# Kernel tuning notes

Hardware: AMD Instinct MI355X
Metric: run time of the kernel (lower is better)

## Reference

```python
import jax, jax.numpy as jnp
import numpy as np

EMBED_DIM = 1024
NUM_HEADS = 16
HEAD_DIM = EMBED_DIM // NUM_HEADS
B, S = 2, 2048
BIG = 1e9  # clamp / nan_to_num saturation value from the torch module


def setup_inputs() -> dict:
    key = jax.random.key(0)
    k1, k2, k3, k4, k5 = jax.random.split(key, 5)
    sc = 1.0 / np.sqrt(EMBED_DIM)
    x = jax.random.normal(k1, (B, S, EMBED_DIM), dtype=jnp.float32)
    qkv_w = jax.random.normal(k2, (3 * EMBED_DIM, EMBED_DIM), dtype=jnp.float32) * sc
    qkv_b = jax.random.normal(k3, (3 * EMBED_DIM,), dtype=jnp.float32) * 0.01
    out_w = jax.random.normal(k4, (EMBED_DIM, EMBED_DIM), dtype=jnp.float32) * sc
    out_b = jax.random.normal(k5, (EMBED_DIM,), dtype=jnp.float32) * 0.01
    # causal mask, broadcastable to [B, H, S, S]; 0 => masked
    mask = jnp.tril(jnp.ones((S, S), dtype=jnp.int32))[None, None, :, :]
    return {"x": x, "mask": mask, "qkv_w": qkv_w, "qkv_b": qkv_b,
            "out_w": out_w, "out_b": out_b}


def reference(x, mask, qkv_w, qkv_b, out_w, out_b):
    b, s, e = x.shape
    # fused QKV projection (torch Linear: x @ W.T + b)
    qkv = x @ qkv_w.T + qkv_b                      # [B, S, 3E]
    q, k, v = jnp.split(qkv, 3, axis=-1)
    def heads(t):
        return t.reshape(b, s, NUM_HEADS, HEAD_DIM).transpose(0, 2, 1, 3)  # [B,H,S,D]
    q, k, v = heads(q), heads(k), heads(v)
    scores = jnp.einsum('bhqd,bhkd->bhqk', q, k) / np.sqrt(HEAD_DIM)
    scores = jnp.clip(scores, -BIG, BIG)
    # masked_fill(mask==0, -inf) then nan_to_num(neginf=-1e9) => masked -> -1e9
    scores = jnp.where(mask == 0, -jnp.inf, scores)
    scores = jnp.nan_to_num(scores, nan=0.0, posinf=BIG, neginf=-BIG)
    scores = scores - jnp.max(scores, axis=-1, keepdims=True)
    attn = jax.nn.softmax(scores, axis=-1) + 1e-9
    out = jnp.einsum('bhqk,bhkd->bhqd', attn, v)   # [B,H,S,D]
    out = out.transpose(0, 2, 1, 3).reshape(b, s, e)
    return out @ out_w.T + out_b
```

## Files before the change

kernel.cpp:

```cpp
#include <hip/hip_runtime.h>
#include <stdint.h>

#define B_ 2
#define H_ 16
#define S_ 2048
#define D_ 64
#define E_ 1024
#define M_ 4096
#define N3_ 3072

typedef __attribute__((ext_vector_type(8))) short bf16x8;
typedef __attribute__((ext_vector_type(4))) float f32x4;
typedef __attribute__((ext_vector_type(16))) float f32x16;
typedef __attribute__((ext_vector_type(4))) unsigned short us4;
typedef __attribute__((ext_vector_type(4))) int i32x4;

__device__ __forceinline__ unsigned short f2b(float f) {
  union { float f; unsigned int u; } v; v.f = f;
  unsigned int r = v.u + 0x7FFFu + ((v.u >> 16) & 1u);
  return (unsigned short)(r >> 16);
}

__device__ __forceinline__ void gll16(const void* g, void* l) {
  __builtin_amdgcn_global_load_lds((const __attribute__((address_space(1))) uint32_t*)g,
                                   (__attribute__((address_space(3))) uint32_t*)l, 16, 0, 0);
}

__global__ __launch_bounds__(256)
void f32_to_bf16_3(const float* __restrict__ a, const float* __restrict__ b,
                   const float* __restrict__ c,
                   unsigned short* __restrict__ oa, unsigned short* __restrict__ ob,
                   unsigned short* __restrict__ oc) {
  int i = (blockIdx.x * blockDim.x + threadIdx.x) * 4;
  const float* src; unsigned short* dst; int j;
  if (i < 4194304)      { src = a; dst = oa; j = i; }
  else if (i < 7340032) { src = b; dst = ob; j = i - 4194304; }
  else                  { src = c; dst = oc; j = i - 7340032; }
  float4 v = *(const float4*)(src + j);
  us4 o; o.x = f2b(v.x); o.y = f2b(v.y); o.z = f2b(v.z); o.w = f2b(v.w);
  *(us4*)(dst + j) = o;
}

template<int MODE>
__global__ __launch_bounds__(512)
void gemm_bt_k(const unsigned short* __restrict__ A,
               const unsigned short* __restrict__ Bw,
               const float* __restrict__ bias,
               float* __restrict__ outf,
               unsigned short* __restrict__ qo,
               unsigned short* __restrict__ ko,
               unsigned short* __restrict__ vto,
               const int K) {
  __shared__ unsigned short As[2][128 * 32];
  __shared__ unsigned short Bs[2][128 * 32];
  const int tid = threadIdx.x;
  const int wid = tid >> 6, lane = tid & 63;
  const int l4 = lane & 15, lh = lane >> 4;
  const int gx = gridDim.x;
  int id = blockIdx.y * gx + blockIdx.x;
  const int cpx = (gx * gridDim.y) >> 3;
  id = (id & 7) * cpx + (id >> 3);
  const int bm = (id / gx) << 7, bn = (id % gx) << 7;
  const int mq = wid >> 2, nq = wid & 3;
  const int wm = mq << 6, wn = nq << 5;
  f32x4 acc[4][2] = {};
  const int srow = lane >> 2;
  const int scolb = ((lane & 3) ^ (((lane >> 3) & 1) << 1)) << 4;
  auto STAGE = [&](int bb, int kt) {
    const int r = (wid << 4) + srow;
    gll16((const char*)A + ((size_t)(bm + r) * K + kt) * 2 + scolb, &As[bb][wid << 9]);
    gll16((const char*)Bw + ((size_t)(bn + r) * K + kt) * 2 + scolb, &Bs[bb][wid << 9]);
  };
  const int NT = K >> 5;
  STAGE(0, 0);
  STAGE(1, 32);
  asm volatile("s_waitcnt vmcnt(2)" ::: "memory");
  __builtin_amdgcn_s_barrier();
  asm volatile("" ::: "memory");
  const int ro = (l4 << 5) + ((lh ^ (((l4 >> 1) & 1) << 1)) << 3);
  for (int t = 0; t < NT; ++t) {
    const int bb = t & 1;
    bf16x8 af[4], bfr[2];
#pragma unroll
    for (int g = 0; g < 4; ++g)
      af[g] = *(const bf16x8*)&As[bb][(((mq << 2) + g) << 9) + ro];
#pragma unroll
    for (int h = 0; h < 2; ++h)
      bfr[h] = *(const bf16x8*)&Bs[bb][(((nq << 1) + h) << 9) + ro];
#pragma unroll
    for (int mg = 0; mg < 4; ++mg)
#pragma unroll
      for (int ng = 0; ng < 2; ++ng)
        acc[mg][ng] = __builtin_amdgcn_mfma_f32_16x16x32_bf16(af[mg], bfr[ng], acc[mg][ng], 0, 0, 0);
    asm volatile("s_waitcnt lgkmcnt(0)" ::: "memory");
    __builtin_amdgcn_s_barrier();
    if (t < NT - 2) {
      STAGE(bb, (t + 2) << 5);
      asm volatile("s_waitcnt vmcnt(2)" ::: "memory");
    } else {
      asm volatile("s_waitcnt vmcnt(0)" ::: "memory");
    }
    __builtin_amdgcn_s_barrier();
    asm volatile("" ::: "memory");
  }
#pragma unroll
  for (int mg = 0; mg < 4; ++mg) {
#pragma unroll
    for (int ng = 0; ng < 2; ++ng) {
      const int n = bn + wn + (ng << 4) + l4;
      const float bv = bias[n];
      const int m0 = bm + wm + (mg << 4) + (lh << 2);
      if (MODE == 1) {
#pragma unroll
        for (int i = 0; i < 4; ++i)
          outf[(size_t)(m0 + i) * E_ + n] = acc[mg][ng][i] + bv;
      } else {
        const int region = n >> 10;
        const int nn = n & 1023;
        const int h = nn >> 6, d = nn & 63;
        const int b = m0 >> 11, s0 = m0 & 2047;
        const int bh = (b << 4) + h;
        if (region == 2) {
          us4 pk;
#pragma unroll
          for (int i = 0; i < 4; ++i) pk[i] = f2b(acc[mg][ng][i] + bv);
          *(us4*)&vto[((size_t)bh * D_ + d) * S_ + s0] = pk;
        } else {
          unsigned short* dst = (region == 0) ? qo : ko;
          const float sc = (region == 0) ? 0.125f : 1.0f;
#pragma unroll
          for (int i = 0; i < 4; ++i)
            dst[((size_t)bh * S_ + s0 + i) * D_ + d] = f2b((acc[mg][ng][i] + bv) * sc);
        }
      }
    }
  }
}

__global__ __launch_bounds__(512)
void attn_k(const unsigned short* __restrict__ Q,
            const unsigned short* __restrict__ Kt,
            const unsigned short* __restrict__ Vt,
            unsigned short* __restrict__ O) {
  __shared__ __align__(16) char smem[65536];
  const int tid = threadIdx.x;
  const int wid = tid >> 6, lane = tid & 63;
  const int l31 = lane & 31, hi = lane >> 5, hi4 = hi << 2;
  const int bid = blockIdx.x;
  const int xcd = bid & 7, jj = bid >> 3;
  const int bh = (xcd << 2) + (jj & 3);
  const int pairq = jj >> 2;
  const int qbB = 15 - pairq;
  const int myqb = (wid < 4) ? pairq : qbB;
  const int q0w = (myqb << 7) + ((wid & 3) << 5);
  const int npair = qbB + 1;
  const int ntaw = ((q0w + 31) >> 6) + 1;

  const char* Qb = (const char*)Q + (size_t)bh * (S_ * D_ * 2);
  const char* Kb = (const char*)Kt + (size_t)bh * (S_ * D_ * 2);
  const char* Vb = (const char*)Vt + (size_t)bh * (D_ * S_ * 2);

  bf16x8 qf[4];
#pragma unroll
  for (int st = 0; st < 4; ++st)
    qf[st] = *(const bf16x8*)(Qb + (size_t)(q0w + l31) * 128 + (st << 5) + (hi << 4));

  const int sw = wid & 3;
  const int r1 = (sw << 4) + (lane >> 3), r2 = r1 + 8;
  const int cc = lane & 7;
  const int ko1 = (r1 << 7) + ((cc ^ (r1 & 7)) << 4);
  const int ko2 = (r2 << 7) + ((cc ^ (r2 & 7)) << 4);
  const int vo1 = (r1 << 12) + ((cc ^ (r1 & 7)) << 4);
  const int vo2 = (r2 << 12) + ((cc ^ (r2 & 7)) << 4);

  f32x16 oacc[2] = {};
  float m_i = -3.0e38f, l_i = 0.0f;
  const int qg = q0w + l31;
  const int swl = l31 & 7;

  auto STAGEP = [&](int b, int tk) {
    const int sub = tk & 1;
    char* kd = smem + (b << 14) + (sub << 13) + (sw << 11);
    char* vd = smem + 32768 + (b << 14) + (sub << 13) + (sw << 11);
    if (wid < 4) {
      gll16(Kb + (size_t)tk * 8192 + ko1, kd);
      gll16(Kb + (size_t)tk * 8192 + ko2, kd + 1024);
    } else {
      gll16(Vb + (size_t)tk * 128 + vo1, vd);
      gll16(Vb + (size_t)tk * 128 + vo2, vd + 1024);
    }
  };

  STAGEP(0, 0); STAGEP(0, 1);
  __syncthreads();

  for (int tp = 0; tp < npair; ++tp) {
    const int cur = tp & 1;
    if (tp + 1 < npair) {
      STAGEP(cur ^ 1, (tp << 1) + 2);
      STAGEP(cur ^ 1, (tp << 1) + 3);
    }
#pragma unroll
    for (int sub = 0; sub < 2; ++sub) {
      const int tk = (tp << 1) + sub;
      if (tk >= ntaw) break;
      const char* Kc = smem + (cur << 14) + (sub << 13);
      const char* Vc = smem + 32768 + (cur << 14) + (sub << 13);
      f32x16 sacc[2] = {};
#pragma unroll
      for (int tt = 0; tt < 2; ++tt)
#pragma unroll
        for (int st = 0; st < 4; ++st) {
          bf16x8 kf = *(const bf16x8*)(Kc + (tt << 12) + (l31 << 7) + ((((st << 1) + hi) ^ swl) << 4));
          sacc[tt] = __builtin_amdgcn_mfma_f32_32x32x16_bf16(kf, qf[st], sacc[tt], 0, 0, 0);
        }
      if (tk == ntaw - 1) {
        const int kv0 = tk << 6;
#pragma unroll
        for (int tt = 0; tt < 2; ++tt)
#pragma unroll
          for (int r = 0; r < 16; ++r) {
            const int kg = kv0 + (tt << 5) + (r & 3) + ((r >> 2) << 3) + hi4;
            if (kg > qg) sacc[tt][r] = -3.0e38f;
          }
      }
      float pmax = -3.0e38f;
#pragma unroll
      for (int tt = 0; tt < 2; ++tt)
#pragma unroll
        for (int r = 0; r < 16; ++r) pmax = fmaxf(pmax, sacc[tt][r]);
      pmax = fmaxf(pmax, __shfl_xor(pmax, 32));
      if (__any(pmax > m_i + 8.0f)) {
        const float mn = fmaxf(m_i, pmax);
        const float scl = __expf(m_i - mn);
        l_i *= scl;
        m_i = mn;
#pragma unroll
        for (int r = 0; r < 16; ++r) {
          const float sr = __shfl(scl, (r & 3) + ((r >> 2) << 3) + hi4);
          oacc[0][r] *= sr;
          oacc[1][r] *= sr;
        }
      }
#pragma unroll
      for (int tt = 0; tt < 2; ++tt)
#pragma unroll
        for (int r = 0; r < 16; ++r) {
          const float p = __expf(sacc[tt][r] - m_i);
          l_i += p;
          sacc[tt][r] = p;
        }
#pragma unroll
      for (int ks = 0; ks < 4; ++ks) {
        const int tt = ks >> 1, r0 = (ks & 1) << 3;
        int w0, w1, w2, w3;
        asm("v_cvt_pk_bf16_f32 %0, %1, %2" : "=v"(w0) : "v"(sacc[tt][r0 + 0]), "v"(sacc[tt][r0 + 1]));
        asm("v_cvt_pk_bf16_f32 %0, %1, %2" : "=v"(w1) : "v"(sacc[tt][r0 + 2]), "v"(sacc[tt][r0 + 3]));
        asm("v_cvt_pk_bf16_f32 %0, %1, %2" : "=v"(w2) : "v"(sacc[tt][r0 + 4]), "v"(sacc[tt][r0 + 5]));
        asm("v_cvt_pk_bf16_f32 %0, %1, %2" : "=v"(w3) : "v"(sacc[tt][r0 + 6]), "v"(sacc[tt][r0 + 7]));
        asm("v_permlane32_swap_b32 %0, %1" : "+v"(w0), "+v"(w2));
        asm("v_permlane32_swap_b32 %0, %1" : "+v"(w1), "+v"(w3));
        union { i32x4 i; bf16x8 h; } u;
        u.i.x = w0; u.i.y = w1; u.i.z = w2; u.i.w = w3;
        const bf16x8 pa = u.h;
#pragma unroll
        for (int dt = 0; dt < 2; ++dt) {
          bf16x8 vf = *(const bf16x8*)(Vc + (dt << 12) + (l31 << 7) + ((((ks << 1) + hi) ^ swl) << 4));
          oacc[dt] = __builtin_amdgcn_mfma_f32_32x32x16_bf16(pa, vf, oacc[dt], 0, 0, 0);
        }
      }
    }
    __syncthreads();
  }

  const float ltot = l_i + __shfl_xor(l_i, 32);
  const float inv = 1.0f / ltot;
  const int b = bh >> 4, h = bh & 15;
#pragma unroll
  for (int r = 0; r < 16; ++r) {
    const int qr = (r & 3) + ((r >> 2) << 3) + hi4;
    const float ivr = __shfl(inv, qr);
    const size_t off = ((size_t)((b << 11) + q0w + qr) << 10) + (h << 6) + l31;
    O[off]      = f2b(oacc[0][r] * ivr);
    O[off + 32] = f2b(oacc[1][r] * ivr);
  }
}

extern "C" void kernel_launch(void* const* d_in, const int* in_sizes, int n_in,
                              void* d_out, int out_size, void* d_ws, size_t ws_size,
                              hipStream_t stream) {
  const float* x     = (const float*)d_in[0];
  const float* qkv_w = (const float*)d_in[2];
  const float* qkv_b = (const float*)d_in[3];
  const float* out_w = (const float*)d_in[4];
  const float* out_b = (const float*)d_in[5];

  unsigned short* ws   = (unsigned short*)d_ws;
  unsigned short* xb   = ws;
  unsigned short* wqkv = xb + (size_t)M_ * E_;
  unsigned short* wout = wqkv + (size_t)N3_ * E_;
  unsigned short* qB   = wout + (size_t)E_ * E_;
  unsigned short* kB   = qB + (size_t)32 * S_ * D_;
  unsigned short* vtB  = kB + (size_t)32 * S_ * D_;
  unsigned short* oB   = ws;

  f32_to_bf16_3<<<8192, 256, 0, stream>>>(x, qkv_w, out_w, xb, wqkv, wout);

  gemm_bt_k<0><<<dim3(N3_ / 128, M_ / 128), 512, 0, stream>>>(
      xb, wqkv, qkv_b, nullptr, qB, kB, vtB, E_);

  attn_k<<<256, 512, 0, stream>>>(qB, kB, vtB, oB);

  gemm_bt_k<1><<<dim3(E_ / 128, M_ / 128), 512, 0, stream>>>(
      oB, wout, out_b, (float*)d_out, nullptr, nullptr, nullptr, E_);
}
```

Before: 106.1 us.

## Store Q/K/V in MFMA-fragment order and load attention operands directly from global

The QKV GEMM epilogue now writes Q, K and V^T in a pre-swizzled fragment layout, so each lane's bf16x8 MFMA operand is a contiguous 16-byte chunk. The attention kernel drops its LDS double-buffering and barriers and reads K/V fragments straight from global/L2 into registers. Blocks shrink to 4 waves with a new per-wave query-tile schedule (heaviest first). This removes LDS traffic and sync costs, but loses cross-wave K/V sharing in LDS and raises register pressure, with K/V loads no longer overlapped with compute by explicit prefetch.

```diff
diff --git a/kernel.cpp b/kernel.cpp
--- a/kernel.cpp
+++ b/kernel.cpp
@@ -124,153 +124,130 @@
           us4 pk;
 #pragma unroll
           for (int i = 0; i < 4; ++i) pk[i] = f2b(acc[mg][ng][i] + bv);
-          *(us4*)&vto[((size_t)bh * D_ + d) * S_ + s0] = pk;
+          const size_t ev = ((size_t)bh << 17) + ((size_t)(s0 >> 6) << 12) + ((d >> 5) << 11)
+                          + (((s0 >> 4) & 3) << 9) + (((s0 >> 3) & 1) << 8)
+                          + ((d & 31) << 3) + (s0 & 7);
+          *(us4*)&vto[ev] = pk;
         } else {
           unsigned short* dst = (region == 0) ? qo : ko;
           const float sc = (region == 0) ? 0.125f : 1.0f;
 #pragma unroll
-          for (int i = 0; i < 4; ++i)
-            dst[((size_t)bh * S_ + s0 + i) * D_ + d] = f2b((acc[mg][ng][i] + bv) * sc);
+          for (int i = 0; i < 4; ++i) {
+            const int s = s0 + i;
+            const size_t e = ((size_t)bh << 17) + ((size_t)(s >> 6) << 12) + (((s >> 5) & 1) << 11)
+                           + ((d >> 4) << 9) + (((d >> 3) & 1) << 8)
+                           + ((s & 31) << 3) + (d & 7);
+            dst[e] = f2b((acc[mg][ng][i] + bv) * sc);
+          }
         }
       }
     }
   }
 }
 
-__global__ __launch_bounds__(512)
-void attn_k(const unsigned short* __restrict__ Q,
-            const unsigned short* __restrict__ Kt,
-            const unsigned short* __restrict__ Vt,
+__global__ __launch_bounds__(256)
+void attn_k(const unsigned short* __restrict__ QF,
+            const unsigned short* __restrict__ KF,
+            const unsigned short* __restrict__ VF,
             unsigned short* __restrict__ O) {
-  __shared__ __align__(16) char smem[65536];
   const int tid = threadIdx.x;
   const int wid = tid >> 6, lane = tid & 63;
   const int l31 = lane & 31, hi = lane >> 5, hi4 = hi << 2;
   const int bid = blockIdx.x;
-  const int xcd = bid & 7, jj = bid >> 3;
-  const int bh = (xcd << 2) + (jj & 3);
-  const int pairq = jj >> 2;
-  const int qbB = 15 - pairq;
-  const int myqb = (wid < 4) ? pairq : qbB;
-  const int q0w = (myqb << 7) + ((wid & 3) << 5);
-  const int npair = qbB + 1;
-  const int ntaw = ((q0w + 31) >> 6) + 1;
-
-  const char* Qb = (const char*)Q + (size_t)bh * (S_ * D_ * 2);
-  const char* Kb = (const char*)Kt + (size_t)bh * (S_ * D_ * 2);
-  const char* Vb = (const char*)Vt + (size_t)bh * (D_ * S_ * 2);
+  const int bh = ((bid & 7) << 2) + ((bid >> 3) & 3);
+  const int qi = 63 - (((bid >> 5) << 2) + wid);
+  const int q0 = qi << 5;
+  const int ntaw = (qi >> 1) + 1;
+
+  const char* Qb = (const char*)QF + ((size_t)bh << 18);
+  const char* Kb = (const char*)KF + ((size_t)bh << 18);
+  const char* Vb = (const char*)VF + ((size_t)bh << 18);
 
   bf16x8 qf[4];
-#pragma unroll
-  for (int st = 0; st < 4; ++st)
-    qf[st] = *(const bf16x8*)(Qb + (size_t)(q0w + l31) * 128 + (st << 5) + (hi << 4));
-
-  const int sw = wid & 3;
-  const int r1 = (sw << 4) + (lane >> 3), r2 = r1 + 8;
-  const int cc = lane & 7;
-  const int ko1 = (r1 << 7) + ((cc ^ (r1 & 7)) << 4);
-  const int ko2 = (r2 << 7) + ((cc ^ (r2 & 7)) << 4);
-  const int vo1 = (r1 << 12) + ((cc ^ (r1 & 7)) << 4);
-  const int vo2 = (r2 << 12) + ((cc ^ (r2 & 7)) << 4);
+  {
+    const char* qc = Qb + ((size_t)(qi >> 1) << 13) + ((qi & 1) << 12) + lane * 16;
+#pragma unroll
+    for (int st = 0; st < 4; ++st)
+      qf[st] = *(const bf16x8*)(qc + (st << 10));
+  }
 
   f32x16 oacc[2] = {};
   float m_i = -3.0e38f, l_i = 0.0f;
-  const int qg = q0w + l31;
-  const int swl = l31 & 7;
-
-  auto STAGEP = [&](int b, int tk) {
-    const int sub = tk & 1;
-    char* kd = smem + (b << 14) + (sub << 13) + (sw << 11);
-    char* vd = smem + 32768 + (b << 14) + (sub << 13) + (sw << 11);
-    if (wid < 4) {
-      gll16(Kb + (size_t)tk * 8192 + ko1, kd);
-      gll16(Kb + (size_t)tk * 8192 + ko2, kd + 1024);
-    } else {
-      gll16(Vb + (size_t)tk * 128 + vo1, vd);
-      gll16(Vb + (size_t)tk * 128 + vo2, vd + 1024);
-    }
-  };
-
-  STAGEP(0, 0); STAGEP(0, 1);
-  __syncthreads();
-
-  for (int tp = 0; tp < npair; ++tp) {
-    const int cur = tp & 1;
-    if (tp + 1 < npair) {
-      STAGEP(cur ^ 1, (tp << 1) + 2);
-      STAGEP(cur ^ 1, (tp << 1) + 3);
-    }
-#pragma unroll
-    for (int sub = 0; sub < 2; ++sub) {
-      const int tk = (tp << 1) + sub;
-      if (tk >= ntaw) break;
-      const char* Kc = smem + (cur << 14) + (sub << 13);
-      const char* Vc = smem + 32768 + (cur << 14) + (sub << 13);
-      f32x16 sacc[2] = {};
+  const int qg = q0 + l31;
+
+  for (int t = 0; t < ntaw; ++t) {
+    const char* Kc = Kb + ((size_t)t << 13) + lane * 16;
+    const char* Vc = Vb + ((size_t)t << 13) + lane * 16;
+    bf16x8 kf[2][4], vf[2][4];
+#pragma unroll
+    for (int tt = 0; tt < 2; ++tt)
+#pragma unroll
+      for (int st = 0; st < 4; ++st)
+        kf[tt][st] = *(const bf16x8*)(Kc + (tt << 12) + (st << 10));
+#pragma unroll
+    for (int dt = 0; dt < 2; ++dt)
+#pragma unroll
+      for (int ks = 0; ks < 4; ++ks)
+        vf[dt][ks] = *(const bf16x8*)(Vc + (dt << 12) + (ks << 10));
+    f32x16 sacc[2] = {};
+#pragma unroll
+    for (int tt = 0; tt < 2; ++tt)
+#pragma unroll
+      for (int st = 0; st < 4; ++st)
+        sacc[tt] = __builtin_amdgcn_mfma_f32_32x32x16_bf16(kf[tt][st], qf[st], sacc[tt], 0, 0, 0);
+    if (t == ntaw - 1) {
+      const int kv0 = t << 6;
 #pragma unroll
       for (int tt = 0; tt < 2; ++tt)
 #pragma unroll
-        for (int st = 0; st < 4; ++st) {
-          bf16x8 kf = *(const bf16x8*)(Kc + (tt << 12) + (l31 << 7) + ((((st << 1) + hi) ^ swl) << 4));
-          sacc[tt] = __builtin_amdgcn_mfma_f32_32x32x16_bf16(kf, qf[st], sacc[tt], 0, 0, 0);
+        for (int r = 0; r < 16; ++r) {
+          const int kg = kv0 + (tt << 5) + (r & 3) + ((r >> 2) << 3) + hi4;
+          if (kg > qg) sacc[tt][r] = -3.0e38f;
         }
-      if (tk == ntaw - 1) {
-        const int kv0 = tk << 6;
-#pragma unroll
-        for (int tt = 0; tt < 2; ++tt)
-#pragma unroll
-          for (int r = 0; r < 16; ++r) {
-            const int kg = kv0 + (tt << 5) + (r & 3) + ((r >> 2) << 3) + hi4;
-            if (kg > qg) sacc[tt][r] = -3.0e38f;
-          }
+    }
+    float pmax = -3.0e38f;
+#pragma unroll
+    for (int tt = 0; tt < 2; ++tt)
+#pragma unroll
+      for (int r = 0; r < 16; ++r) pmax = fmaxf(pmax, sacc[tt][r]);
+    pmax = fmaxf(pmax, __shfl_xor(pmax, 32));
+    if (__any(pmax > m_i + 8.0f)) {
+      const float mn = fmaxf(m_i, pmax);
+      const float scl = __expf(m_i - mn);
+      l_i *= scl;
+      m_i = mn;
+#pragma unroll
+      for (int r = 0; r < 16; ++r) {
+        const float sr = __shfl(scl, (r & 3) + ((r >> 2) << 3) + hi4);
+        oacc[0][r] *= sr;
+        oacc[1][r] *= sr;
       }
-      float pmax = -3.0e38f;
-#pragma unroll
-      for (int tt = 0; tt < 2; ++tt)
-#pragma unroll
-        for (int r = 0; r < 16; ++r) pmax = fmaxf(pmax, sacc[tt][r]);
-      pmax = fmaxf(pmax, __shfl_xor(pmax, 32));
-      if (__any(pmax > m_i + 8.0f)) {
-        const float mn = fmaxf(m_i, pmax);
-        const float scl = __expf(m_i - mn);
-        l_i *= scl;
-        m_i = mn;
-#pragma unroll
-        for (int r = 0; r < 16; ++r) {
-          const float sr = __shfl(scl, (r & 3) + ((r >> 2) << 3) + hi4);
-          oacc[0][r] *= sr;
-          oacc[1][r] *= sr;
-        }
+    }
+#pragma unroll
+    for (int tt = 0; tt < 2; ++tt)
+#pragma unroll
+      for (int r = 0; r < 16; ++r) {
+        const float p = __expf(sacc[tt][r] - m_i);
+        l_i += p;
+        sacc[tt][r] = p;
       }
 #pragma unroll
-      for (int tt = 0; tt < 2; ++tt)
-#pragma unroll
-        for (int r = 0; r < 16; ++r) {
-          const float p = __expf(sacc[tt][r] - m_i);
-          l_i += p;
-          sacc[tt][r] = p;
-        }
-#pragma unroll
-      for (int ks = 0; ks < 4; ++ks) {
-        const int tt = ks >> 1, r0 = (ks & 1) << 3;
-        int w0, w1, w2, w3;
-        asm("v_cvt_pk_bf16_f32 %0, %1, %2" : "=v"(w0) : "v"(sacc[tt][r0 + 0]), "v"(sacc[tt][r0 + 1]));
-        asm("v_cvt_pk_bf16_f32 %0, %1, %2" : "=v"(w1) : "v"(sacc[tt][r0 + 2]), "v"(sacc[tt][r0 + 3]));
-        asm("v_cvt_pk_bf16_f32 %0, %1, %2" : "=v"(w2) : "v"(sacc[tt][r0 + 4]), "v"(sacc[tt][r0 + 5]));
-        asm("v_cvt_pk_bf16_f32 %0, %1, %2" : "=v"(w3) : "v"(sacc[tt][r0 + 6]), "v"(sacc[tt][r0 + 7]));
-        asm("v_permlane32_swap_b32 %0, %1" : "+v"(w0), "+v"(w2));
-        asm("v_permlane32_swap_b32 %0, %1" : "+v"(w1), "+v"(w3));
-        union { i32x4 i; bf16x8 h; } u;
-        u.i.x = w0; u.i.y = w1; u.i.z = w2; u.i.w = w3;
-        const bf16x8 pa = u.h;
-#pragma unroll
-        for (int dt = 0; dt < 2; ++dt) {
-          bf16x8 vf = *(const bf16x8*)(Vc + (dt << 12) + (l31 << 7) + ((((ks << 1) + hi) ^ swl) << 4));
-          oacc[dt] = __builtin_amdgcn_mfma_f32_32x32x16_bf16(pa, vf, oacc[dt], 0, 0, 0);
-        }
-      }
-    }
-    __syncthreads();
+    for (int ks = 0; ks < 4; ++ks) {
+      const int tt = ks >> 1, r0 = (ks & 1) << 3;
+      int w0, w1, w2, w3;
+      asm("v_cvt_pk_bf16_f32 %0, %1, %2" : "=v"(w0) : "v"(sacc[tt][r0 + 0]), "v"(sacc[tt][r0 + 1]));
+      asm("v_cvt_pk_bf16_f32 %0, %1, %2" : "=v"(w1) : "v"(sacc[tt][r0 + 2]), "v"(sacc[tt][r0 + 3]));
+      asm("v_cvt_pk_bf16_f32 %0, %1, %2" : "=v"(w2) : "v"(sacc[tt][r0 + 4]), "v"(sacc[tt][r0 + 5]));
+      asm("v_cvt_pk_bf16_f32 %0, %1, %2" : "=v"(w3) : "v"(sacc[tt][r0 + 6]), "v"(sacc[tt][r0 + 7]));
+      asm("v_permlane32_swap_b32 %0, %1" : "+v"(w0), "+v"(w2));
+      asm("v_permlane32_swap_b32 %0, %1" : "+v"(w1), "+v"(w3));
+      union { i32x4 i; bf16x8 h; } u;
+      u.i.x = w0; u.i.y = w1; u.i.z = w2; u.i.w = w3;
+      const bf16x8 pa = u.h;
+#pragma unroll
+      for (int dt = 0; dt < 2; ++dt)
+        oacc[dt] = __builtin_amdgcn_mfma_f32_32x32x16_bf16(pa, vf[dt][ks], oacc[dt], 0, 0, 0);
+    }
   }
 
   const float ltot = l_i + __shfl_xor(l_i, 32);
@@ -280,7 +257,7 @@
   for (int r = 0; r < 16; ++r) {
     const int qr = (r & 3) + ((r >> 2) << 3) + hi4;
     const float ivr = __shfl(inv, qr);
-    const size_t off = ((size_t)((b << 11) + q0w + qr) << 10) + (h << 6) + l31;
+    const size_t off = ((size_t)((b << 11) + q0 + qr) << 10) + (h << 6) + l31;
     O[off]      = f2b(oacc[0][r] * ivr);
     O[off + 32] = f2b(oacc[1][r] * ivr);
   }
@@ -309,7 +286,7 @@
   gemm_bt_k<0><<<dim3(N3_ / 128, M_ / 128), 512, 0, stream>>>(
       xb, wqkv, qkv_b, nullptr, qB, kB, vtB, E_);
 
-  attn_k<<<256, 512, 0, stream>>>(qB, kB, vtB, oB);
+  attn_k<<<512, 256, 0, stream>>>(qB, kB, vtB, oB);
 
   gemm_bt_k<1><<<dim3(E_ / 128, M_ / 128), 512, 0, stream>>>(
       oB, wout, out_b, (float*)d_out, nullptr, nullptr, nullptr, E_);
```

After: 121.0 us. 1.14x slower.
